# Optimization experiments

Measured on AMD Instinct MI355X. Metric: run time of the kernel, lower is better.

The kernel has to match this reference:

```python
import jax, jax.numpy as jnp
import numpy as np

N_NODES = 6890
N_ANGLES = 8
K_CHEB = 15
N_DESC = 544
HIDDEN = 64
N_CLASS = 6890
M = N_ANGLES * N_NODES  # 55120, size of anisotropic Laplacian
DEG = 16
NNZ = M * DEG
BN_EPS = 1e-5


def setup_inputs() -> dict:
    key = jax.random.key(0)
    ks = jax.random.split(key, 16)
    x = jax.random.normal(ks[0], (N_NODES, N_DESC), dtype=jnp.float32)
    # sparse anisotropic Laplacian (M x M), ~DEG nnz per row
    rows = jnp.repeat(jnp.arange(M, dtype=jnp.int32), DEG)
    cols = jax.random.randint(ks[1], (NNZ,), 0, M, dtype=jnp.int32)
    vals = jax.random.normal(ks[2], (NNZ,), dtype=jnp.float32) * 0.1
    # conv1: (K, n_angles*n_desc, 64); conv2..6 stacked: (5, K, n_angles*64, 64)
    def xavier(k, shape, fan_in, fan_out):
        lim = np.sqrt(6.0 / (fan_in + fan_out))
        return jax.random.uniform(k, shape, jnp.float32, -lim, lim)
    W1 = xavier(ks[3], (K_CHEB, N_ANGLES * N_DESC, HIDDEN), N_ANGLES * N_DESC, HIDDEN)
    Wc = xavier(ks[4], (5, K_CHEB, N_ANGLES * HIDDEN, HIDDEN), N_ANGLES * HIDDEN, HIDDEN)
    conv_b = jnp.zeros((6, HIDDEN), jnp.float32)
    bn_gamma = jnp.ones((6, HIDDEN), jnp.float32)
    bn_beta = jnp.zeros((6, HIDDEN), jnp.float32)
    fc2_w = xavier(ks[5], (HIDDEN, 256), HIDDEN, 256)
    fc2_b = jnp.zeros((256,), jnp.float32)
    fc3_w = xavier(ks[6], (256, N_CLASS), 256, N_CLASS)
    fc3_b = jnp.zeros((N_CLASS,), jnp.float32)
    return {"x": x, "rows": rows, "cols": cols, "vals": vals,
            "W1": W1, "Wc": Wc, "conv_b": conv_b,
            "bn_gamma": bn_gamma, "bn_beta": bn_beta,
            "fc2_w": fc2_w, "fc2_b": fc2_b, "fc3_w": fc3_w, "fc3_b": fc3_b}


def _spmm(rows, cols, vals, T):
    # (M x M sparse) @ (M x C) via gather + segment-sum
    return jax.ops.segment_sum(vals[:, None] * T[cols], rows, num_segments=M)


def _acs_conv(x, rows, cols, vals, W, b):
    # x: (N, C). Chebyshev recurrence on the (A*N, C) angle-stacked signal.
    N, C = x.shape
    A = N_ANGLES

    def proj(T, Wk):
        # (A*N, C) -> (N, A*C) @ (A*C, out)
        return T.reshape(A, N, C).transpose(1, 0, 2).reshape(N, A * C) @ Wk

    T0 = jnp.tile(x, (A, 1))
    out = proj(T0, W[0])
    T1 = _spmm(rows, cols, vals, T0)
    out = out + proj(T1, W[1])
    for k in range(2, K_CHEB):
        T2 = 2.0 * _spmm(rows, cols, vals, T1) - T0
        out = out + proj(T2, W[k])
        T0, T1 = T1, T2
    return out + b


def _bn_relu(x, gamma, beta):
    # BatchNorm1d (training-mode batch stats, biased variance) + ReLU
    mean = jnp.mean(x, axis=0)
    var = jnp.var(x, axis=0)
    return jax.nn.relu((x - mean) * jax.lax.rsqrt(var + BN_EPS) * gamma + beta)


def reference(x, rows, cols, vals, W1, Wc, conv_b, bn_gamma, bn_beta,
              fc2_w, fc2_b, fc3_w, fc3_b):
    h = _bn_relu(_acs_conv(x, rows, cols, vals, W1, conv_b[0]), bn_gamma[0], bn_beta[0])
    for i in range(5):
        h = _bn_relu(_acs_conv(h, rows, cols, vals, Wc[i], conv_b[i + 1]),
                     bn_gamma[i + 1], bn_beta[i + 1])
    h = jax.nn.relu(h @ fc2_w + fc2_b)
    # dropout is identity at inference
    return h @ fc3_w + fc3_b
```

## Files before the change

kernel.cpp:

```cpp
#include <hip/hip_runtime.h>
#include <cstdint>
#include <cstddef>

#define NN 6890
#define NA 8
#define KC 15
#define ND 544
#define MR (NA * NN)
#define DEG 16
#define NNZ (MR * DEG)
#define BN_EPS 1e-5f
#define NRG 108
#define PB (NA * NRG)

typedef unsigned int u32;
typedef _Float16 f16;
typedef __attribute__((ext_vector_type(8))) _Float16 f16x8;
typedef __attribute__((ext_vector_type(4))) float f32x4;

union U4H8 { uint4 q; f16 h[8]; f16x8 v; };

__device__ __forceinline__ u32 packh(float a, float b) {
    union { f16 h[2]; u32 u; } c;
    c.h[0] = (f16)a; c.h[1] = (f16)b; return c.u;
}
__device__ __forceinline__ uint4 pack8h(const float* t) {
    uint4 m;
    m.x = packh(t[0], t[1]); m.y = packh(t[2], t[3]);
    m.z = packh(t[4], t[5]); m.w = packh(t[6], t[7]);
    return m;
}
__device__ __forceinline__ void acc8h(float* s, float v, uint4 g) {
    U4H8 c; c.q = g;
    #pragma unroll
    for (int i = 0; i < 8; ++i) s[i] += v * (float)c.h[i];
}

__global__ __launch_bounds__(256)
void prep_cv_kernel(const int* __restrict__ cols, const float* __restrict__ vals,
                    uint4* __restrict__ cvq)
{
    const int q = blockIdx.x * 256 + threadIdx.x;
    if (q >= NNZ / 4) return;
    const int4   c = ((const int4*)cols)[q];
    const float4 v = ((const float4*)vals)[q];
    uint4 o;
    o.x = ((u32)c.x & 0xffffu) | ((u32)c.y << 16);
    o.y = ((u32)c.z & 0xffffu) | ((u32)c.w << 16);
    o.z = packh(v.x, v.y);
    o.w = packh(v.z, v.w);
    cvq[q] = o;
}

template<int CC>
__global__ __launch_bounds__(256)
void tile_slab_kernel(const float* __restrict__ X, int C_in, int c0,
                      uint4* __restrict__ slab0)
{
    constexpr int LPR = CC / 8;
    constexpr int RPB = 256 / LPR;
    const int tid = threadIdx.x;
    const int j = tid % LPR, rloc = tid / LPR;
    const int r = blockIdx.x * RPB + rloc;
    if (r >= MR) return;
    const int n = r % NN;
    const float* xp = X + (size_t)n * C_in + c0 + 8 * j;
    const float4 t0 = *(const float4*)xp;
    const float4 t1 = *(const float4*)(xp + 4);
    float t[8] = { t0.x, t0.y, t0.z, t0.w, t1.x, t1.y, t1.z, t1.w };
    slab0[(size_t)r * LPR + j] = pack8h(t);
}

template<int CC, bool CHEB>
__device__ __forceinline__
void spmm_body(const uint4* __restrict__ sp, const uint4* __restrict__ sc,
               uint4* __restrict__ sw, const uint4* __restrict__ cvq)
{
    constexpr int LPR = CC / 8;
    constexpr int RPB = 256 / LPR;
    const int tid = threadIdx.x;
    const int j = tid % LPR, rloc = tid / LPR;
    const int r = blockIdx.x * RPB + rloc;
    if (r >= MR) return;

    int c[16]; float v[16];
    const uint4* cvp = cvq + (size_t)r * 4;
    #pragma unroll
    for (int q = 0; q < 4; ++q) {
        const uint4 cq = cvp[q];
        c[4 * q + 0] = cq.x & 0xffffu; c[4 * q + 1] = cq.x >> 16;
        c[4 * q + 2] = cq.y & 0xffffu; c[4 * q + 3] = cq.y >> 16;
        union { u32 u; f16 h[2]; } z, w_;
        z.u = cq.z; w_.u = cq.w;
        v[4 * q + 0] = (float)z.h[0]; v[4 * q + 1] = (float)z.h[1];
        v[4 * q + 2] = (float)w_.h[0]; v[4 * q + 3] = (float)w_.h[1];
    }
    float s[8] = {0.f, 0.f, 0.f, 0.f, 0.f, 0.f, 0.f, 0.f};
    #pragma unroll
    for (int d = 0; d < DEG; ++d)
        acc8h(s, v[d], sp[(size_t)c[d] * LPR + j]);
    float t[8];
    if (CHEB) {
        U4H8 p; p.q = sc[(size_t)r * LPR + j];
        #pragma unroll
        for (int i = 0; i < 8; ++i) t[i] = 2.f * s[i] - (float)p.h[i];
    } else {
        #pragma unroll
        for (int i = 0; i < 8; ++i) t[i] = s[i];
    }
    sw[(size_t)r * LPR + j] = pack8h(t);
}

template<int CC, bool CHEB>
__global__ __launch_bounds__(256)
void spmm_only_kernel(const uint4* __restrict__ sp, const uint4* __restrict__ sc,
                      uint4* __restrict__ sw, const uint4* __restrict__ cvq)
{
    spmm_body<CC, CHEB>(sp, sc, sw, cvq);
}

template<int CC, int NPROJ, bool FIRSTP>
__device__ __forceinline__
void proj_body(int pb, const uint4* __restrict__ s0, const uint4* __restrict__ s1,
               const float* __restrict__ W, float* __restrict__ part,
               int C_in, int c0, int kbase, u32* WH, u32* WL)
{
    constexpr int CCH = CC / 32;
    constexpr int LPR = CC / 8;
    const int tid = threadIdx.x;
    const int l = tid & 63, w = tid >> 6;
    const int a = pb / NRG, rg = pb % NRG;
    const int rows0 = rg * 64;
    const int hi16 = l >> 4;

    const int arow = rows0 + w * 16 + (l & 15);
    const int arc  = arow < NN ? arow : NN - 1;
    const size_t abase = (size_t)(a * NN + arc) * LPR;

    f32x4 acc[4];
    #pragma unroll
    for (int nt = 0; nt < 4; ++nt) {
        #pragma unroll
        for (int rr = 0; rr < 4; ++rr) {
            const int orow = rows0 + w * 16 + hi16 * 4 + rr;
            float vv = 0.f;
            if (!FIRSTP && orow < NN)
                vv = part[((size_t)a * NN + orow) * 64 + nt * 16 + (l & 15)];
            acc[nt][rr] = vv;
        }
    }

    #pragma unroll
    for (int p = 0; p < NPROJ; ++p) {
        const uint4* sl = (p == 0) ? s0 : s1;
        const float* Wk = W + ((size_t)(kbase + p) * NA * C_in + (size_t)a * C_in + c0) * 64;
        if (p) __syncthreads();
        for (int e = tid; e < CCH * 1024; e += 256) {
            const int i2 = e & 3;
            const int ll = (e >> 2) & 63;
            const int nt = (e >> 8) & 3;
            const int h  = e >> 10;
            const int cc  = h * 32 + (ll >> 4) * 8 + 2 * i2;
            const int col = nt * 16 + (ll & 15);
            const float w0 = Wk[(size_t)cc * 64 + col];
            const float w1 = Wk[(size_t)(cc + 1) * 64 + col];
            const f16 h0 = (f16)w0, h1 = (f16)w1;
            union { f16 h[2]; u32 u; } ph, pl;
            ph.h[0] = h0; ph.h[1] = h1;
            pl.h[0] = (f16)(w0 - (float)h0); pl.h[1] = (f16)(w1 - (float)h1);
            WH[e] = ph.u; WL[e] = pl.u;
        }
        __syncthreads();
        #pragma unroll
        for (int h = 0; h < CCH; ++h) {
            U4H8 af; af.q = sl[abase + h * 4 + hi16];
            #pragma unroll
            for (int nt = 0; nt < 4; ++nt) {
                const int be = ((h * 4 + nt) * 64 + l) * 4;
                U4H8 bh, bl;
                bh.q = *(const uint4*)&WH[be];
                bl.q = *(const uint4*)&WL[be];
                acc[nt] = __builtin_amdgcn_mfma_f32_16x16x32_f16(af.v, bh.v, acc[nt], 0, 0, 0);
                acc[nt] = __builtin_amdgcn_mfma_f32_16x16x32_f16(af.v, bl.v, acc[nt], 0, 0, 0);
            }
        }
    }

    #pragma unroll
    for (int nt = 0; nt < 4; ++nt) {
        #pragma unroll
        for (int rr = 0; rr < 4; ++rr) {
            const int orow = rows0 + w * 16 + hi16 * 4 + rr;
            if (orow < NN)
                part[((size_t)a * NN + orow) * 64 + nt * 16 + (l & 15)] = acc[nt][rr];
        }
    }
}

template<int CC, bool FIRSTP>
__global__ __launch_bounds__(256)
void step2_kernel(const uint4* __restrict__ sp, const uint4* __restrict__ sc,
                  uint4* __restrict__ sw, const uint4* __restrict__ cvq,
                  const float* __restrict__ W, float* __restrict__ part,
                  int C_in, int c0, int kbase, int NB)
{
    constexpr int CCH = CC / 32;
    __shared__ u32 WH[CCH * 1024];
    __shared__ u32 WL[CCH * 1024];
    if ((int)blockIdx.x < NB)
        spmm_body<CC, true>(sp, sc, sw, cvq);
    else
        proj_body<CC, 2, FIRSTP>((int)blockIdx.x - NB, sc, sp, W, part, C_in, c0, kbase, WH, WL);
}

template<int CC>
__global__ __launch_bounds__(256)
void proj_final_kernel(const uint4* __restrict__ sl, const float* __restrict__ W,
                       float* __restrict__ part, int C_in, int c0, int kproj)
{
    constexpr int CCH = CC / 32;
    __shared__ u32 WH[CCH * 1024];
    __shared__ u32 WL[CCH * 1024];
    proj_body<CC, 1, false>((int)blockIdx.x, sl, sl, W, part, C_in, c0, kproj, WH, WL);
}

__global__ void bn_reduce_kernel(const float* __restrict__ part, float* __restrict__ acc)
{
    const int e = blockIdx.x * blockDim.x + threadIdx.x;
    if (e >= NN * 64) return;
    float s = 0.f;
    #pragma unroll
    for (int a = 0; a < NA; ++a) s += part[(size_t)a * NN * 64 + e];
    acc[e] = s;
}

__global__ __launch_bounds__(256)
void bn_stats_kernel(const float* __restrict__ acc, const float* __restrict__ gamma,
                     const float* __restrict__ beta, float* __restrict__ bnp)
{
    const int h = blockIdx.x;
    float s = 0.f, sq = 0.f;
    for (int n = threadIdx.x; n < NN; n += 256) {
        const float v = acc[(size_t)n * 64 + h];
        s += v; sq += v * v;
    }
    __shared__ float ls[256], lq[256];
    ls[threadIdx.x] = s; lq[threadIdx.x] = sq;
    __syncthreads();
    for (int st = 128; st > 0; st >>= 1) {
        if (threadIdx.x < st) { ls[threadIdx.x] += ls[threadIdx.x + st]; lq[threadIdx.x] += lq[threadIdx.x + st]; }
        __syncthreads();
    }
    if (threadIdx.x == 0) {
        const float mean = ls[0] / (float)NN;
        const float var  = lq[0] / (float)NN - mean * mean;
        const float sc   = gamma[h] / sqrtf(var + BN_EPS);
        bnp[h]      = sc;
        bnp[64 + h] = beta[h] - mean * sc;
    }
}

__global__ void bn_apply_kernel(const float* __restrict__ acc, const float* __restrict__ bnp,
                                float* __restrict__ H)
{
    const int e = blockIdx.x * blockDim.x + threadIdx.x;
    if (e >= NN * 64) return;
    const int h = e & 63;
    const float v = acc[e] * bnp[h] + bnp[64 + h];
    H[e] = v > 0.f ? v : 0.f;
}

template<bool RELU>
__global__ __launch_bounds__(256)
void gemm_bias_kernel(const float* __restrict__ A, const float* __restrict__ B,
                      const float* __restrict__ bias, float* __restrict__ C,
                      int Mm, int Nn, int Kk)
{
    __shared__ float As[16][132];
    __shared__ float Bs[16][132];
    const int tx = threadIdx.x & 15, ty = threadIdx.x >> 4;
    const int m0 = blockIdx.y * 128, n0 = blockIdx.x * 128;
    const bool full = (m0 + 128 <= Mm) && (n0 + 128 <= Nn);
    float acc[8][8] = {};
    for (int k0 = 0; k0 < Kk; k0 += 16) {
        if (full) {
            #pragma unroll
            for (int e = threadIdx.x; e < 512; e += 256) {
                const int i = e >> 2, q = e & 3;
                const float4 a4 = *(const float4*)&A[(size_t)(m0 + i) * Kk + k0 + 4 * q];
                As[4 * q + 0][i] = a4.x; As[4 * q + 1][i] = a4.y;
                As[4 * q + 2][i] = a4.z; As[4 * q + 3][i] = a4.w;
            }
            #pragma unroll
            for (int e = threadIdx.x; e < 512; e += 256) {
                const int kk = e >> 5, q = e & 31;
                *(float4*)&Bs[kk][4 * q] = *(const float4*)&B[(size_t)(k0 + kk) * Nn + n0 + 4 * q];
            }
        } else {
            for (int e = threadIdx.x; e < 128 * 16; e += 256) {
                const int i = e >> 4, kk = e & 15;
                const int row = m0 + i;
                As[kk][i] = (row < Mm) ? A[(size_t)row * Kk + k0 + kk] : 0.f;
            }
            for (int e = threadIdx.x; e < 16 * 128; e += 256) {
                const int kk = e >> 7, jj = e & 127;
                const int col = n0 + jj;
                Bs[kk][jj] = (col < Nn) ? B[(size_t)(k0 + kk) * Nn + col] : 0.f;
            }
        }
        __syncthreads();
        #pragma unroll
        for (int kk = 0; kk < 16; ++kk) {
            float av[8], bv[8];
            *(float4*)&av[0] = *(const float4*)&As[kk][ty * 4];
            *(float4*)&av[4] = *(const float4*)&As[kk][64 + ty * 4];
            *(float4*)&bv[0] = *(const float4*)&Bs[kk][tx * 4];
            *(float4*)&bv[4] = *(const float4*)&Bs[kk][64 + tx * 4];
            #pragma unroll
            for (int i = 0; i < 8; ++i)
                #pragma unroll
                for (int jj = 0; jj < 8; ++jj)
                    acc[i][jj] += av[i] * bv[jj];
        }
        __syncthreads();
    }
    for (int i = 0; i < 8; ++i) {
        const int row = m0 + (i < 4 ? ty * 4 + i : 64 + ty * 4 + (i - 4));
        if (row >= Mm) continue;
        for (int jj = 0; jj < 8; ++jj) {
            const int col = n0 + (jj < 4 ? tx * 4 + jj : 64 + tx * 4 + (jj - 4));
            if (col >= Nn) continue;
            float v = acc[i][jj] + bias[col];
            if (RELU) v = fmaxf(v, 0.f);
            C[(size_t)row * Nn + col] = v;
        }
    }
}

__global__ __launch_bounds__(256)
void w3_split_kernel(const float* __restrict__ W, f16* __restrict__ Wh, f16* __restrict__ Wl)
{
    __shared__ float t[64][65];
    const int tid = threadIdx.x;
    const int n0 = blockIdx.x * 64, k0 = blockIdx.y * 64;
    for (int e = tid; e < 64 * 64; e += 256) {
        const int kk = e >> 6, nn = e & 63;
        const int gn = n0 + nn;
        t[kk][nn] = (gn < NN) ? W[(size_t)(k0 + kk) * NN + gn] : 0.f;
    }
    __syncthreads();
    for (int e = tid; e < 64 * 8; e += 256) {
        const int nn = e >> 3, c8 = e & 7;
        const int gn = n0 + nn;
        if (gn >= NN) continue;
        const size_t ob = ((size_t)((k0 >> 3) + c8) * NN + gn) * 8;
        f16 vh[8], vl[8];
        #pragma unroll
        for (int i = 0; i < 8; ++i) {
            const float w = t[c8 * 8 + i][nn];
            const f16 h = (f16)w;
            vh[i] = h; vl[i] = (f16)(w - (float)h);
        }
        *(uint4*)&Wh[ob] = *(const uint4*)vh;
        *(uint4*)&Wl[ob] = *(const uint4*)vl;
    }
}

__global__ __launch_bounds__(256)
void f2_split_kernel(const float* __restrict__ f2, f16* __restrict__ Ah, f16* __restrict__ Al)
{
    const int row = blockIdx.x * 256 + threadIdx.x;
    const int c = blockIdx.y;
    if (row >= NN) return;
    const float4 a0 = *(const float4*)&f2[(size_t)row * 256 + c * 8];
    const float4 a1 = *(const float4*)&f2[(size_t)row * 256 + c * 8 + 4];
    const float vv[8] = { a0.x, a0.y, a0.z, a0.w, a1.x, a1.y, a1.z, a1.w };
    f16 vh[8], vl[8];
    #pragma unroll
    for (int i = 0; i < 8; ++i) {
        const f16 h = (f16)vv[i];
        vh[i] = h; vl[i] = (f16)(vv[i] - (float)h);
    }
    const size_t ob = ((size_t)c * NN + row) * 8;
    *(uint4*)&Ah[ob] = *(const uint4*)vh;
    *(uint4*)&Al[ob] = *(const uint4*)vl;
}

__global__ __launch_bounds__(256)
void fc3_mfma_kernel(const f16* __restrict__ Ah, const f16* __restrict__ Al,
                     const f16* __restrict__ Bh, const f16* __restrict__ Bl,
                     const float* __restrict__ bias, float* __restrict__ C)
{
    const int tid = threadIdx.x, l = tid & 63, w = tid >> 6;
    const int wm = w >> 1, wn = w & 1, hi16 = l >> 4;
    const int m0 = blockIdx.y * 128, n0 = blockIdx.x * 128;

    size_t aoff[4], boff[4];
    #pragma unroll
    for (int mf = 0; mf < 4; ++mf) {
        int row = m0 + wm * 64 + mf * 16 + (l & 15);
        if (row > NN - 1) row = NN - 1;
        aoff[mf] = (size_t)row * 8;
    }
    #pragma unroll
    for (int nf = 0; nf < 4; ++nf) {
        int col = n0 + wn * 64 + nf * 16 + (l & 15);
        if (col > NN - 1) col = NN - 1;
        boff[nf] = (size_t)col * 8;
    }

    f32x4 acc[4][4];
    #pragma unroll
    for (int mf = 0; mf < 4; ++mf)
        #pragma unroll
        for (int nf = 0; nf < 4; ++nf)
            acc[mf][nf] = (f32x4){0.f, 0.f, 0.f, 0.f};

    for (int k0 = 0; k0 < 256; k0 += 32) {
        const size_t cb = (size_t)((k0 >> 3) + hi16) * NN * 8;
        f16x8 ah[4], al[4], bh[4], bl[4];
        #pragma unroll
        for (int mf = 0; mf < 4; ++mf) {
            ah[mf] = *(const f16x8*)(Ah + cb + aoff[mf]);
            al[mf] = *(const f16x8*)(Al + cb + aoff[mf]);
        }
        #pragma unroll
        for (int nf = 0; nf < 4; ++nf) {
            bh[nf] = *(const f16x8*)(Bh + cb + boff[nf]);
            bl[nf] = *(const f16x8*)(Bl + cb + boff[nf]);
        }
        #pragma unroll
        for (int mf = 0; mf < 4; ++mf)
            #pragma unroll
            for (int nf = 0; nf < 4; ++nf) {
                acc[mf][nf] = __builtin_amdgcn_mfma_f32_16x16x32_f16(ah[mf], bh[nf], acc[mf][nf], 0, 0, 0);
                acc[mf][nf] = __builtin_amdgcn_mfma_f32_16x16x32_f16(ah[mf], bl[nf], acc[mf][nf], 0, 0, 0);
                acc[mf][nf] = __builtin_amdgcn_mfma_f32_16x16x32_f16(al[mf], bh[nf], acc[mf][nf], 0, 0, 0);
            }
    }

    #pragma unroll
    for (int mf = 0; mf < 4; ++mf) {
        #pragma unroll
        for (int nf = 0; nf < 4; ++nf) {
            const int col = n0 + wn * 64 + nf * 16 + (l & 15);
            if (col >= NN) continue;
            const float bv = bias[col];
            #pragma unroll
            for (int rr = 0; rr < 4; ++rr) {
                const int row = m0 + wm * 64 + mf * 16 + hi16 * 4 + rr;
                if (row < NN)
                    C[(size_t)row * NN + col] = acc[mf][nf][rr] + bv;
            }
        }
    }
}

template<int CC>
static void run_chunk(bool first, const float* X, int C_in, int c0,
                      const uint4* cvq, const float* W,
                      uint4* const sl[4], float* part, hipStream_t stream)
{
    constexpr int RPB = 256 / (CC / 8);
    const int NB = (MR + RPB - 1) / RPB;

    tile_slab_kernel<CC><<<NB, 256, 0, stream>>>(X, C_in, c0, sl[0]);
    spmm_only_kernel<CC, false><<<NB, 256, 0, stream>>>(sl[0], sl[0], sl[1], cvq);
    for (int k = 2; k < KC; ++k) {
        const int p = (k - 1) & 3, c = (k - 2) & 3, n = k & 3;
        if (k & 1) {
            spmm_only_kernel<CC, true><<<NB, 256, 0, stream>>>(sl[p], sl[c], sl[n], cvq);
        } else {
            if (first && k == 2)
                step2_kernel<CC, true ><<<NB + PB, 256, 0, stream>>>(
                    sl[p], sl[c], sl[n], cvq, W, part, C_in, c0, k - 2, NB);
            else
                step2_kernel<CC, false><<<NB + PB, 256, 0, stream>>>(
                    sl[p], sl[c], sl[n], cvq, W, part, C_in, c0, k - 2, NB);
        }
    }
    proj_final_kernel<CC><<<PB, 256, 0, stream>>>(sl[(KC - 1) & 3], W, part, C_in, c0, KC - 1);
}

extern "C" void kernel_launch(void* const* d_in, const int* in_sizes, int n_in,
                              void* d_out, int out_size, void* d_ws, size_t ws_size,
                              hipStream_t stream)
{
    (void)in_sizes; (void)n_in; (void)out_size; (void)ws_size;
    const float* x     = (const float*)d_in[0];
    const int*   cols  = (const int*)  d_in[2];
    const float* vals  = (const float*)d_in[3];
    const float* W1    = (const float*)d_in[4];
    const float* Wc    = (const float*)d_in[5];
    const float* gamma = (const float*)d_in[7];
    const float* beta  = (const float*)d_in[8];
    const float* fc2w  = (const float*)d_in[9];
    const float* fc2b  = (const float*)d_in[10];
    const float* fc3w  = (const float*)d_in[11];
    const float* fc3b  = (const float*)d_in[12];

    const size_t MT   = (size_t)MR * 64;
    const size_t SLOT = (size_t)MR * 8;

    char* base = (char*)d_ws;
    size_t off = 0;
    uint4* cvq  = (uint4*)(base + off); off += (size_t)(NNZ / 4) * 16;
    uint4* slabs = (uint4*)(base + off); off += 4 * SLOT * 16;
    float* part = (float*)(base + off); off += MT * 4;
    float* acc  = (float*)(base + off); off += (size_t)NN * 64 * 4;
    float* H    = (float*)(base + off); off += (size_t)NN * 64 * 4;
    float* f2   = (float*)(base + off); off += (size_t)NN * 256 * 4;
    f16* f2h    = (f16*)(base + off);   off += (size_t)NN * 256 * 2;
    f16* f2l    = (f16*)(base + off);   off += (size_t)NN * 256 * 2;
    f16* W3h    = (f16*)(base + off);   off += (size_t)NN * 256 * 2;
    f16* W3l    = (f16*)(base + off);   off += (size_t)NN * 256 * 2;
    float* bnp  = (float*)(base + off);

    uint4* sl[4] = { slabs, slabs + SLOT, slabs + 2 * SLOT, slabs + 3 * SLOT };

    prep_cv_kernel<<<(NNZ / 4 + 255) / 256, 256, 0, stream>>>(cols, vals, cvq);
    w3_split_kernel<<<dim3(108, 4), 256, 0, stream>>>(fc3w, W3h, W3l);

    for (int li = 0; li < 6; ++li) {
        const int C_in = (li == 0) ? ND : 64;
        const float* X = (li == 0) ? x : H;
        const float* W = (li == 0) ? W1 : Wc + (size_t)(li - 1) * KC * (NA * 64) * 64;
        const int nfull = C_in / 64;
        for (int c = 0; c < nfull; ++c)
            run_chunk<64>(c == 0, X, C_in, c * 64, cvq, W, sl, part, stream);
        if (C_in % 64)
            run_chunk<32>(false, X, C_in, nfull * 64, cvq, W, sl, part, stream);

        bn_reduce_kernel<<<(NN * 64 + 255) / 256, 256, 0, stream>>>(part, acc);
        bn_stats_kernel<<<64, 256, 0, stream>>>(acc, gamma + li * 64, beta + li * 64, bnp);
        bn_apply_kernel<<<(NN * 64 + 255) / 256, 256, 0, stream>>>(acc, bnp, H);
    }

    gemm_bias_kernel<true><<<dim3(2, 54), 256, 0, stream>>>(H, fc2w, fc2b, f2, NN, 256, 64);
    f2_split_kernel<<<dim3(27, 32), 256, 0, stream>>>(f2, f2h, f2l);
    fc3_mfma_kernel<<<dim3(54, 54), 256, 0, stream>>>(f2h, f2l, W3h, W3l, fc3b, (float*)d_out);
}
```

Before: 4.292 ms.

## Widen first-layer channel chunks, stage sparse index rows in LDS, use 3-slot ring

The first layer's 544 input channels are now processed in wider chunks (256 or 128 channels, chosen by available workspace) instead of eight 64-channel chunks. This cuts the number of full 15-step Chebyshev passes, so the sparse column/value index stream is read far fewer times. The projection kernel loops over 64-channel slices of each wide slab so its weight staging in shared memory stays the same size. SpMM blocks also copy their rows' packed index/value entries into shared memory first, and the slab ring drops from 4 to 3 slots so wider slabs fit in the workspace. Wider rows use more memory per gathered row and have fewer blocks, which may hurt cache hit rate for the random gathers.

Measured after the change: 4.172 ms. 1.03x faster.

```diff
diff --git a/kernel.cpp b/kernel.cpp
--- a/kernel.cpp
+++ b/kernel.cpp
@@ -74,20 +74,25 @@
 template<int CC, bool CHEB>
 __device__ __forceinline__
 void spmm_body(const uint4* __restrict__ sp, const uint4* __restrict__ sc,
-               uint4* __restrict__ sw, const uint4* __restrict__ cvq)
+               uint4* __restrict__ sw, const uint4* __restrict__ cvq,
+               uint4* cvl)
 {
     constexpr int LPR = CC / 8;
     constexpr int RPB = 256 / LPR;
     const int tid = threadIdx.x;
     const int j = tid % LPR, rloc = tid / LPR;
-    const int r = blockIdx.x * RPB + rloc;
+    const int r0 = blockIdx.x * RPB;
+    const int nrow = (MR - r0) < RPB ? (MR - r0) : RPB;
+    for (int e = tid; e < nrow * 4; e += 256)
+        cvl[e] = cvq[(size_t)r0 * 4 + e];
+    __syncthreads();
+    const int r = r0 + rloc;
     if (r >= MR) return;
 
     int c[16]; float v[16];
-    const uint4* cvp = cvq + (size_t)r * 4;
     #pragma unroll
     for (int q = 0; q < 4; ++q) {
-        const uint4 cq = cvp[q];
+        const uint4 cq = cvl[rloc * 4 + q];
         c[4 * q + 0] = cq.x & 0xffffu; c[4 * q + 1] = cq.x >> 16;
         c[4 * q + 2] = cq.y & 0xffffu; c[4 * q + 3] = cq.y >> 16;
         union { u32 u; f16 h[2]; } z, w_;
@@ -116,17 +121,21 @@
 void spmm_only_kernel(const uint4* __restrict__ sp, const uint4* __restrict__ sc,
                       uint4* __restrict__ sw, const uint4* __restrict__ cvq)
 {
-    spmm_body<CC, CHEB>(sp, sc, sw, cvq);
-}
-
-template<int CC, int NPROJ, bool FIRSTP>
+    constexpr int RPB = 256 / (CC / 8);
+    __shared__ uint4 cvl[RPB * 4];
+    spmm_body<CC, CHEB>(sp, sc, sw, cvq, cvl);
+}
+
+template<int SCC, int NPROJ, bool FIRSTP>
 __device__ __forceinline__
 void proj_body(int pb, const uint4* __restrict__ s0, const uint4* __restrict__ s1,
                const float* __restrict__ W, float* __restrict__ part,
                int C_in, int c0, int kbase, u32* WH, u32* WL)
 {
-    constexpr int CCH = CC / 32;
-    constexpr int LPR = CC / 8;
+    constexpr int LPRF   = SCC / 8;
+    constexpr int SLICES = SCC >= 64 ? SCC / 64 : 1;
+    constexpr int SCH    = SCC >= 64 ? 64 : SCC;
+    constexpr int CCH    = SCH / 32;
     const int tid = threadIdx.x;
     const int l = tid & 63, w = tid >> 6;
     const int a = pb / NRG, rg = pb % NRG;
@@ -135,7 +144,7 @@
 
     const int arow = rows0 + w * 16 + (l & 15);
     const int arc  = arow < NN ? arow : NN - 1;
-    const size_t abase = (size_t)(a * NN + arc) * LPR;
+    const size_t abase = (size_t)(a * NN + arc) * LPRF;
 
     f32x4 acc[4];
     #pragma unroll
@@ -153,35 +162,39 @@
     #pragma unroll
     for (int p = 0; p < NPROJ; ++p) {
         const uint4* sl = (p == 0) ? s0 : s1;
-        const float* Wk = W + ((size_t)(kbase + p) * NA * C_in + (size_t)a * C_in + c0) * 64;
-        if (p) __syncthreads();
-        for (int e = tid; e < CCH * 1024; e += 256) {
-            const int i2 = e & 3;
-            const int ll = (e >> 2) & 63;
-            const int nt = (e >> 8) & 3;
-            const int h  = e >> 10;
-            const int cc  = h * 32 + (ll >> 4) * 8 + 2 * i2;
-            const int col = nt * 16 + (ll & 15);
-            const float w0 = Wk[(size_t)cc * 64 + col];
-            const float w1 = Wk[(size_t)(cc + 1) * 64 + col];
-            const f16 h0 = (f16)w0, h1 = (f16)w1;
-            union { f16 h[2]; u32 u; } ph, pl;
-            ph.h[0] = h0; ph.h[1] = h1;
-            pl.h[0] = (f16)(w0 - (float)h0); pl.h[1] = (f16)(w1 - (float)h1);
-            WH[e] = ph.u; WL[e] = pl.u;
-        }
-        __syncthreads();
-        #pragma unroll
-        for (int h = 0; h < CCH; ++h) {
-            U4H8 af; af.q = sl[abase + h * 4 + hi16];
+        #pragma unroll
+        for (int s = 0; s < SLICES; ++s) {
+            const float* Wk = W + ((size_t)(kbase + p) * NA * C_in
+                                   + (size_t)a * C_in + c0 + s * 64) * 64;
+            if (p | s) __syncthreads();
+            for (int e = tid; e < CCH * 1024; e += 256) {
+                const int i2 = e & 3;
+                const int ll = (e >> 2) & 63;
+                const int nt = (e >> 8) & 3;
+                const int h  = e >> 10;
+                const int cc  = h * 32 + (ll >> 4) * 8 + 2 * i2;
+                const int col = nt * 16 + (ll & 15);
+                const float w0 = Wk[(size_t)cc * 64 + col];
+                const float w1 = Wk[(size_t)(cc + 1) * 64 + col];
+                const f16 h0 = (f16)w0, h1 = (f16)w1;
+                union { f16 h[2]; u32 u; } ph, pl;
+                ph.h[0] = h0; ph.h[1] = h1;
+                pl.h[0] = (f16)(w0 - (float)h0); pl.h[1] = (f16)(w1 - (float)h1);
+                WH[e] = ph.u; WL[e] = pl.u;
+            }
+            __syncthreads();
             #pragma unroll
-            for (int nt = 0; nt < 4; ++nt) {
-                const int be = ((h * 4 + nt) * 64 + l) * 4;
-                U4H8 bh, bl;
-                bh.q = *(const uint4*)&WH[be];
-                bl.q = *(const uint4*)&WL[be];
-                acc[nt] = __builtin_amdgcn_mfma_f32_16x16x32_f16(af.v, bh.v, acc[nt], 0, 0, 0);
-                acc[nt] = __builtin_amdgcn_mfma_f32_16x16x32_f16(af.v, bl.v, acc[nt], 0, 0, 0);
+            for (int h = 0; h < CCH; ++h) {
+                U4H8 af; af.q = sl[abase + s * 8 + h * 4 + hi16];
+                #pragma unroll
+                for (int nt = 0; nt < 4; ++nt) {
+                    const int be = ((h * 4 + nt) * 64 + l) * 4;
+                    U4H8 bh, bl;
+                    bh.q = *(const uint4*)&WH[be];
+                    bl.q = *(const uint4*)&WL[be];
+                    acc[nt] = __builtin_amdgcn_mfma_f32_16x16x32_f16(af.v, bh.v, acc[nt], 0, 0, 0);
+                    acc[nt] = __builtin_amdgcn_mfma_f32_16x16x32_f16(af.v, bl.v, acc[nt], 0, 0, 0);
+                }
             }
         }
     }
@@ -204,11 +217,12 @@
                   const float* __restrict__ W, float* __restrict__ part,
                   int C_in, int c0, int kbase, int NB)
 {
-    constexpr int CCH = CC / 32;
-    __shared__ u32 WH[CCH * 1024];
-    __shared__ u32 WL[CCH * 1024];
+    constexpr int RPB = 256 / (CC / 8);
+    __shared__ uint4 cvl[RPB * 4];
+    __shared__ u32 WH[2048];
+    __shared__ u32 WL[2048];
     if ((int)blockIdx.x < NB)
-        spmm_body<CC, true>(sp, sc, sw, cvq);
+        spmm_body<CC, true>(sp, sc, sw, cvq, cvl);
     else
         proj_body<CC, 2, FIRSTP>((int)blockIdx.x - NB, sc, sp, W, part, C_in, c0, kbase, WH, WL);
 }
@@ -218,9 +232,8 @@
 void proj_final_kernel(const uint4* __restrict__ sl, const float* __restrict__ W,
                        float* __restrict__ part, int C_in, int c0, int kproj)
 {
-    constexpr int CCH = CC / 32;
-    __shared__ u32 WH[CCH * 1024];
-    __shared__ u32 WL[CCH * 1024];
+    __shared__ u32 WH[2048];
+    __shared__ u32 WL[2048];
     proj_body<CC, 1, false>((int)blockIdx.x, sl, sl, W, part, C_in, c0, kproj, WH, WL);
 }
 
@@ -459,15 +472,17 @@
 template<int CC>
 static void run_chunk(bool first, const float* X, int C_in, int c0,
                       const uint4* cvq, const float* W,
-                      uint4* const sl[4], float* part, hipStream_t stream)
+                      uint4* slabs, float* part, hipStream_t stream)
 {
     constexpr int RPB = 256 / (CC / 8);
     const int NB = (MR + RPB - 1) / RPB;
+    const size_t SLOT = (size_t)MR * (CC / 8);
+    uint4* sl[3] = { slabs, slabs + SLOT, slabs + 2 * SLOT };
 
     tile_slab_kernel<CC><<<NB, 256, 0, stream>>>(X, C_in, c0, sl[0]);
     spmm_only_kernel<CC, false><<<NB, 256, 0, stream>>>(sl[0], sl[0], sl[1], cvq);
     for (int k = 2; k < KC; ++k) {
-        const int p = (k - 1) & 3, c = (k - 2) & 3, n = k & 3;
+        const int p = (k - 1) % 3, c = (k - 2) % 3, n = k % 3;
         if (k & 1) {
             spmm_only_kernel<CC, true><<<NB, 256, 0, stream>>>(sl[p], sl[c], sl[n], cvq);
         } else {
@@ -479,14 +494,14 @@
                     sl[p], sl[c], sl[n], cvq, W, part, C_in, c0, k - 2, NB);
         }
     }
-    proj_final_kernel<CC><<<PB, 256, 0, stream>>>(sl[(KC - 1) & 3], W, part, C_in, c0, KC - 1);
+    proj_final_kernel<CC><<<PB, 256, 0, stream>>>(sl[(KC - 1) % 3], W, part, C_in, c0, KC - 1);
 }
 
 extern "C" void kernel_launch(void* const* d_in, const int* in_sizes, int n_in,
                               void* d_out, int out_size, void* d_ws, size_t ws_size,
                               hipStream_t stream)
 {
-    (void)in_sizes; (void)n_in; (void)out_size; (void)ws_size;
+    (void)in_sizes; (void)n_in; (void)out_size;
     const float* x     = (const float*)d_in[0];
     const int*   cols  = (const int*)  d_in[2];
     const float* vals  = (const float*)d_in[3];
@@ -499,13 +514,25 @@
     const float* fc3w  = (const float*)d_in[11];
     const float* fc3b  = (const float*)d_in[12];
 
-    const size_t MT   = (size_t)MR * 64;
-    const size_t SLOT = (size_t)MR * 8;
+    const size_t MT = (size_t)MR * 64;
+    const size_t FIXED = (size_t)(NNZ / 4) * 16
+                       + MT * 4
+                       + (size_t)NN * 64 * 4 * 2
+                       + (size_t)NN * 256 * 4
+                       + (size_t)NN * 256 * 2 * 4
+                       + 1024;
+    const size_t ring256 = 3 * (size_t)MR * 512;
+    const size_t ring128 = 3 * (size_t)MR * 256;
+    const size_t ring64  = 3 * (size_t)MR * 128;
+    int ccL0 = 64;
+    size_t ring = ring64;
+    if (ws_size >= FIXED + ring256)      { ccL0 = 256; ring = ring256; }
+    else if (ws_size >= FIXED + ring128) { ccL0 = 128; ring = ring128; }
 
     char* base = (char*)d_ws;
     size_t off = 0;
     uint4* cvq  = (uint4*)(base + off); off += (size_t)(NNZ / 4) * 16;
-    uint4* slabs = (uint4*)(base + off); off += 4 * SLOT * 16;
+    uint4* slabs = (uint4*)(base + off); off += ring;
     float* part = (float*)(base + off); off += MT * 4;
     float* acc  = (float*)(base + off); off += (size_t)NN * 64 * 4;
     float* H    = (float*)(base + off); off += (size_t)NN * 64 * 4;
@@ -516,8 +543,6 @@
     f16* W3l    = (f16*)(base + off);   off += (size_t)NN * 256 * 2;
     float* bnp  = (float*)(base + off);
 
-    uint4* sl[4] = { slabs, slabs + SLOT, slabs + 2 * SLOT, slabs + 3 * SLOT };
-
     prep_cv_kernel<<<(NNZ / 4 + 255) / 256, 256, 0, stream>>>(cols, vals, cvq);
     w3_split_kernel<<<dim3(108, 4), 256, 0, stream>>>(fc3w, W3h, W3l);
 
@@ -525,11 +550,25 @@
         const int C_in = (li == 0) ? ND : 64;
         const float* X = (li == 0) ? x : H;
         const float* W = (li == 0) ? W1 : Wc + (size_t)(li - 1) * KC * (NA * 64) * 64;
-        const int nfull = C_in / 64;
-        for (int c = 0; c < nfull; ++c)
-            run_chunk<64>(c == 0, X, C_in, c * 64, cvq, W, sl, part, stream);
-        if (C_in % 64)
-            run_chunk<32>(false, X, C_in, nfull * 64, cvq, W, sl, part, stream);
+
+        if (li == 0) {
+            int c0 = 0;
+            bool first = true;
+            const int wide = ccL0;
+            while (c0 + wide <= 512) {
+                if (wide == 256)      run_chunk<256>(first, X, C_in, c0, cvq, W, slabs, part, stream);
+                else if (wide == 128) run_chunk<128>(first, X, C_in, c0, cvq, W, slabs, part, stream);
+                else                  run_chunk<64> (first, X, C_in, c0, cvq, W, slabs, part, stream);
+                c0 += wide; first = false;
+            }
+            while (c0 + 64 <= ND) {
+                run_chunk<64>(first, X, C_in, c0, cvq, W, slabs, part, stream);
+                c0 += 64; first = false;
+            }
+            run_chunk<32>(false, X, C_in, c0, cvq, W, slabs, part, stream);
+        } else {
+            run_chunk<64>(true, X, C_in, 0, cvq, W, slabs, part, stream);
+        }
 
         bn_reduce_kernel<<<(NN * 64 + 255) / 256, 256, 0, stream>>>(part, acc);
         bn_stats_kernel<<<64, 256, 0, stream>>>(acc, gamma + li * 64, beta + li * 64, bnp);
```
